# Kernel tuning notes

Measured on AMD Instinct MI355X. Metric: run time of the kernel, lower is better.

The kernel has to match this reference:

```python
import jax, jax.numpy as jnp
import numpy as np


def setup_inputs() -> dict:
    key = jax.random.key(0)
    # coeffs_tensor: stacked/padded wavelet coefficients [B, F, T]
    coeffs = jax.random.normal(key, (16, 256, 8192), dtype=jnp.float32)
    return {"coeffs": coeffs}


def reference(coeffs) -> jnp.ndarray:
    B, F, T = coeffs.shape
    # torch.angle on a real tensor -> 0 for x>=0, pi for x<0; jnp.angle matches.
    phase = jnp.angle(coeffs)
    inst_freq = jnp.diff(phase, axis=-1)
    inst_freq = jnp.pad(inst_freq, ((0, 0), (0, 0), (0, 1)))  # F.pad(..., (0,1))
    freq_adjusted = jnp.clip(inst_freq, -1.0, 1.0)  # [B,F,T]
    # k = (f + freq_adjusted).long(); .long() truncates toward zero, as does astype(int32)
    f_idx = jnp.arange(F, dtype=coeffs.dtype)[None, :, None]
    k = jnp.clip((f_idx + freq_adjusted).astype(jnp.int32), 0, F - 1)  # [B,F,T]
    # Fused scatter-add over all (b, f, t): sst[b, k[b,f,t], t] += coeffs[b, f, t]
    b_idx = jnp.arange(B)[:, None, None]
    t_idx = jnp.arange(T)[None, None, :]
    sst = jnp.zeros_like(coeffs).at[b_idx, k, t_idx].add(coeffs)
    return sst
```

## Files before the change

kernel.cpp:

```cpp
#include <hip/hip_runtime.h>

typedef float f32x4 __attribute__((ext_vector_type(4)));

#define BB 16
#define FF 256
#define TT 8192
#define F_CHUNK 8
#define ROWS (F_CHUNK + 2)
#define THREADS 256
#define TBLK (THREADS * 4)
#define NXBLK (TT / TBLK)
#define LROW 1024

__device__ __forceinline__ void dma16(const float* g, float* l) {
    __builtin_amdgcn_global_load_lds(
        (const __attribute__((address_space(1))) unsigned int*)g,
        (__attribute__((address_space(3))) unsigned int*)l,
        16, 0, 0);
}

__device__ __forceinline__ int sgn_bit(float x) {
    return (int)(__float_as_uint(x) >> 31);
}

__global__ __launch_bounds__(THREADS) void sst_kernel(const float* __restrict__ in,
                                                      float* __restrict__ out) {
    __shared__ float sm[ROWS][LROW];

    const int tid    = threadIdx.x;
    const int wid    = tid >> 6;
    const int tid4   = tid * 4;
    const int blockT = blockIdx.x * TBLK;
    const int fs     = blockIdx.y * F_CHUNK;
    const int b      = blockIdx.z;

    const float* srcRow = in  + (size_t)b * FF * TT;
    float*       dstRow = out + (size_t)b * FF * TT;

    #pragma unroll
    for (int i = 0; i < ROWS; ++i) {
        int f = fs - 1 + i;
        f = f < 0 ? 0 : (f > FF - 1 ? FF - 1 : f);
        dma16(srcRow + (size_t)f * TT + blockT + tid4, &sm[i][wid * 256]);
        __builtin_amdgcn_sched_barrier(0);
    }

    const int  eidx    = (tid4 + 4 > LROW - 1) ? (LROW - 1) : (tid4 + 4);
    const bool tailThr = (blockIdx.x == NXBLK - 1) && (tid == THREADS - 1);

    f32x4    v[ROWS];
    unsigned pk[ROWS];

    auto finish_row = [&](int i) {
        v[i] = *reinterpret_cast<const f32x4*>(&sm[i][tid4]);
        const float e = sm[i][eidx];
        const int f   = fs - 1 + i;
        const bool oob = (f < 0) | (f > FF - 1);
        const int s0 = sgn_bit(v[i][0]), s1 = sgn_bit(v[i][1]),
                  s2 = sgn_bit(v[i][2]), s3 = sgn_bit(v[i][3]), s4 = sgn_bit(e);
        const int a0 = s1 - s0 + 1, a1 = s2 - s1 + 1, a2 = s3 - s2 + 1;
        const int a3 = tailThr ? 1 : (s4 - s3 + 1);
        pk[i] = oob ? 0x55u : (unsigned)(a0 | (a1 << 2) | (a2 << 4) | (a3 << 6));
    };

    auto emit_row = [&](int i) {
        const int g = fs + (i - 1);
        const bool isFirst = (g == 0), isLast = (g == FF - 1);
        const unsigned pp = pk[i - 1], pc = pk[i], pn = pk[i + 1];
        const f32x4    vp = v[i - 1],  vc = v[i],  vn = v[i + 1];
        f32x4 r;
        #pragma unroll
        for (int q = 0; q < 4; ++q) {
            const unsigned cp = (pp >> (2 * q)) & 3u;
            const unsigned cc = (pc >> (2 * q)) & 3u;
            const unsigned cn = (pn >> (2 * q)) & 3u;
            const bool bc = (cc == 1u) || (isFirst && cc == 0u) || (isLast && cc == 2u);
            r[q] = ((cp == 2u) ? vp[q] : 0.f) + (bc ? vc[q] : 0.f) + ((cn == 0u) ? vn[q] : 0.f);
        }
        __builtin_nontemporal_store(
            r, reinterpret_cast<f32x4*>(dstRow + (size_t)g * TT + blockT + tid4));
    };

    asm volatile("s_waitcnt vmcnt(6)" ::: "memory");
    __builtin_amdgcn_s_barrier();
    __builtin_amdgcn_sched_barrier(0);
    finish_row(0); finish_row(1); finish_row(2); finish_row(3);
    emit_row(1); emit_row(2);

    asm volatile("s_waitcnt vmcnt(5)" ::: "memory");
    __builtin_amdgcn_s_barrier();
    __builtin_amdgcn_sched_barrier(0);
    finish_row(4); finish_row(5); finish_row(6);
    emit_row(3); emit_row(4); emit_row(5);

    asm volatile("s_waitcnt vmcnt(5)" ::: "memory");
    __builtin_amdgcn_s_barrier();
    __builtin_amdgcn_sched_barrier(0);
    finish_row(7); finish_row(8); finish_row(9);
    emit_row(6); emit_row(7); emit_row(8);

    if (blockIdx.x != NXBLK - 1) {
        asm volatile("s_waitcnt vmcnt(0)" ::: "memory");
        __builtin_amdgcn_s_barrier();
        __builtin_amdgcn_sched_barrier(0);
        if (tid < F_CHUNK) {
            const int g = fs + tid;
            const size_t cg = (size_t)(blockT + TBLK - 1);
            const float vpv = sm[tid][LROW - 1];
            const float vcv = sm[tid + 1][LROW - 1];
            const float vnv = sm[tid + 2][LROW - 1];
            const float* nc = srcRow + cg + 1;
            const int am = (g - 1 >= 0)
                         ? (sgn_bit(nc[(size_t)(g - 1) * TT]) - sgn_bit(vpv)) : 9;
            const int ac =  sgn_bit(nc[(size_t)g * TT]) - sgn_bit(vcv);
            const int an = (g + 1 <= FF - 1)
                         ? (sgn_bit(nc[(size_t)(g + 1) * TT]) - sgn_bit(vnv)) : 9;
            const bool bcb = (ac == 0) || (g == 0 && ac < 0) || (g == FF - 1 && ac > 0);
            float r = 0.f;
            if (am == 1)  r += vpv;
            if (bcb)      r += vcv;
            if (an == -1) r += vnv;
            dstRow[(size_t)g * TT + cg] = r;
        }
    }
}

extern "C" void kernel_launch(void* const* d_in, const int* in_sizes, int n_in,
                              void* d_out, int out_size, void* d_ws, size_t ws_size,
                              hipStream_t stream) {
    const float* in  = (const float*)d_in[0];
    float*       out = (float*)d_out;
    dim3 grid(NXBLK, FF / F_CHUNK, BB);
    sst_kernel<<<grid, THREADS, 0, stream>>>(in, out);
}
```

Measured before the change: 228.6 us.

## Halve time tile to 512 with 2-wide vectors and single wait

Shrinks each block's time tile from 1024 to 512 columns, so each thread handles 2 floats instead of 4 and LDS use per block halves. It adds a minBlocksPerCU launch bound of 8 to raise occupancy. The staged partial vmcnt waits are replaced by one full wait before compute. The intent is more resident blocks to hide memory latency, at the cost of twice as many blocks, more halo reloads per output, narrower stores and loss of the load/compute overlap inside a block.

```diff
diff --git a/kernel.cpp b/kernel.cpp
--- a/kernel.cpp
+++ b/kernel.cpp
@@ -1,6 +1,6 @@
 #include <hip/hip_runtime.h>
 
-typedef float f32x4 __attribute__((ext_vector_type(4)));
+typedef float f32x2 __attribute__((ext_vector_type(2)));
 
 #define BB 16
 #define FF 256
@@ -8,9 +8,9 @@
 #define F_CHUNK 8
 #define ROWS (F_CHUNK + 2)
 #define THREADS 256
-#define TBLK (THREADS * 4)
+#define TBLK 512
 #define NXBLK (TT / TBLK)
-#define LROW 1024
+#define LROW 512
 
 __device__ __forceinline__ void dma16(const float* g, float* l) {
     __builtin_amdgcn_global_load_lds(
@@ -23,13 +23,13 @@
     return (int)(__float_as_uint(x) >> 31);
 }
 
-__global__ __launch_bounds__(THREADS) void sst_kernel(const float* __restrict__ in,
-                                                      float* __restrict__ out) {
+__global__ __launch_bounds__(THREADS, 8) void sst_kernel(const float* __restrict__ in,
+                                                         float* __restrict__ out) {
     __shared__ float sm[ROWS][LROW];
 
     const int tid    = threadIdx.x;
     const int wid    = tid >> 6;
-    const int tid4   = tid * 4;
+    const int lane   = tid & 63;
     const int blockT = blockIdx.x * TBLK;
     const int fs     = blockIdx.y * F_CHUNK;
     const int b      = blockIdx.z;
@@ -38,39 +38,47 @@
     float*       dstRow = out + (size_t)b * FF * TT;
 
     #pragma unroll
-    for (int i = 0; i < ROWS; ++i) {
-        int f = fs - 1 + i;
+    for (int s = 0; s < ROWS / 2; ++s) {
+        const int row  = s * 2 + (wid >> 1);
+        const int half = wid & 1;
+        int f = fs - 1 + row;
         f = f < 0 ? 0 : (f > FF - 1 ? FF - 1 : f);
-        dma16(srcRow + (size_t)f * TT + blockT + tid4, &sm[i][wid * 256]);
-        __builtin_amdgcn_sched_barrier(0);
+        dma16(srcRow + (size_t)f * TT + blockT + half * 256 + lane * 4,
+              &sm[row][half * 256]);
     }
 
-    const int  eidx    = (tid4 + 4 > LROW - 1) ? (LROW - 1) : (tid4 + 4);
+    asm volatile("s_waitcnt vmcnt(0)" ::: "memory");
+    __builtin_amdgcn_s_barrier();
+    __builtin_amdgcn_sched_barrier(0);
+
+    const int  tid2    = tid * 2;
+    const int  eidx    = (tid2 + 2 > LROW - 1) ? (LROW - 1) : (tid2 + 2);
     const bool tailThr = (blockIdx.x == NXBLK - 1) && (tid == THREADS - 1);
 
-    f32x4    v[ROWS];
+    f32x2    v[ROWS];
     unsigned pk[ROWS];
 
-    auto finish_row = [&](int i) {
-        v[i] = *reinterpret_cast<const f32x4*>(&sm[i][tid4]);
+    #pragma unroll
+    for (int i = 0; i < ROWS; ++i) {
+        v[i] = *reinterpret_cast<const f32x2*>(&sm[i][tid2]);
         const float e = sm[i][eidx];
         const int f   = fs - 1 + i;
         const bool oob = (f < 0) | (f > FF - 1);
-        const int s0 = sgn_bit(v[i][0]), s1 = sgn_bit(v[i][1]),
-                  s2 = sgn_bit(v[i][2]), s3 = sgn_bit(v[i][3]), s4 = sgn_bit(e);
-        const int a0 = s1 - s0 + 1, a1 = s2 - s1 + 1, a2 = s3 - s2 + 1;
-        const int a3 = tailThr ? 1 : (s4 - s3 + 1);
-        pk[i] = oob ? 0x55u : (unsigned)(a0 | (a1 << 2) | (a2 << 4) | (a3 << 6));
-    };
+        const int s0 = sgn_bit(v[i][0]), s1 = sgn_bit(v[i][1]), s2 = sgn_bit(e);
+        const int a0 = s1 - s0 + 1;
+        const int a1 = tailThr ? 1 : (s2 - s1 + 1);
+        pk[i] = oob ? 0x5u : (unsigned)(a0 | (a1 << 2));
+    }
 
-    auto emit_row = [&](int i) {
+    #pragma unroll
+    for (int i = 1; i <= F_CHUNK; ++i) {
         const int g = fs + (i - 1);
         const bool isFirst = (g == 0), isLast = (g == FF - 1);
         const unsigned pp = pk[i - 1], pc = pk[i], pn = pk[i + 1];
-        const f32x4    vp = v[i - 1],  vc = v[i],  vn = v[i + 1];
-        f32x4 r;
+        const f32x2    vp = v[i - 1],  vc = v[i],  vn = v[i + 1];
+        f32x2 r;
         #pragma unroll
-        for (int q = 0; q < 4; ++q) {
+        for (int q = 0; q < 2; ++q) {
             const unsigned cp = (pp >> (2 * q)) & 3u;
             const unsigned cc = (pc >> (2 * q)) & 3u;
             const unsigned cn = (pn >> (2 * q)) & 3u;
@@ -78,26 +86,8 @@
             r[q] = ((cp == 2u) ? vp[q] : 0.f) + (bc ? vc[q] : 0.f) + ((cn == 0u) ? vn[q] : 0.f);
         }
         __builtin_nontemporal_store(
-            r, reinterpret_cast<f32x4*>(dstRow + (size_t)g * TT + blockT + tid4));
-    };
-
-    asm volatile("s_waitcnt vmcnt(6)" ::: "memory");
-    __builtin_amdgcn_s_barrier();
-    __builtin_amdgcn_sched_barrier(0);
-    finish_row(0); finish_row(1); finish_row(2); finish_row(3);
-    emit_row(1); emit_row(2);
-
-    asm volatile("s_waitcnt vmcnt(5)" ::: "memory");
-    __builtin_amdgcn_s_barrier();
-    __builtin_amdgcn_sched_barrier(0);
-    finish_row(4); finish_row(5); finish_row(6);
-    emit_row(3); emit_row(4); emit_row(5);
-
-    asm volatile("s_waitcnt vmcnt(5)" ::: "memory");
-    __builtin_amdgcn_s_barrier();
-    __builtin_amdgcn_sched_barrier(0);
-    finish_row(7); finish_row(8); finish_row(9);
-    emit_row(6); emit_row(7); emit_row(8);
+            r, reinterpret_cast<f32x2*>(dstRow + (size_t)g * TT + blockT + tid2));
+    }
 
     if (blockIdx.x != NXBLK - 1) {
         asm volatile("s_waitcnt vmcnt(0)" ::: "memory");
```

After: 229.3 us. Within noise of the previous version (+0.3%).
